# Performance work log

Hardware: AMD Instinct MI355X
Metric: run time of the kernel (lower is better)

Reference implementation:

```python
import jax, jax.numpy as jnp
import numpy as np

RANKS_HIGH = 15   # dt.RANKS.HIGH in the repo
SUITS_HIGH = 14   # padded so conv output last dim == 10 (Linear(10,32))
EPS = 1e-5


def _bn(x, g, b, axes):
    # Batch-norm over `axes` with channel dim = 1, training-mode batch stats.
    m = jnp.mean(x, axis=axes, keepdims=True)
    v = jnp.var(x, axis=axes, keepdims=True)
    xn = (x - m) * jax.lax.rsqrt(v + EPS)
    shp = [1] * x.ndim
    shp[1] = -1
    return xn * g.reshape(shp) + b.reshape(shp)


def setup_inputs() -> dict:
    key = jax.random.key(0)
    ks = jax.random.split(key, 16)
    M = 4096
    s = 0.05
    return {
        "x": jax.random.randint(ks[0], (M, 5, 2), 0, 4),  # (rank, suit) indices
        "conv_w": jax.random.normal(ks[1], (64, 5, 5, 5), jnp.float32) * s,
        "conv_b": jax.random.normal(ks[2], (64,), jnp.float32) * s,
        "bn0_g": jnp.ones((64,), jnp.float32),
        "bn0_b": jnp.zeros((64,), jnp.float32),
        "w_rank": jax.random.normal(ks[3], (32, 10), jnp.float32) * s,
        "b_rank": jax.random.normal(ks[4], (32,), jnp.float32) * s,
        "w_h1": jax.random.normal(ks[5], (32, 32), jnp.float32) * s,
        "b_h1": jax.random.normal(ks[6], (32,), jnp.float32) * s,
        "bn1_g": jnp.ones((64,), jnp.float32),
        "bn1_b": jnp.zeros((64,), jnp.float32),
        "w_h2": jax.random.normal(ks[7], (16, 32), jnp.float32) * s,
        "b_h2": jax.random.normal(ks[8], (16,), jnp.float32) * s,
        "bn2_g": jnp.ones((64,), jnp.float32),
        "bn2_b": jnp.zeros((64,), jnp.float32),
        "w_out": jax.random.normal(ks[9], (9, 11264), jnp.float32) * s,
        "b_out": jax.random.normal(ks[10], (9,), jnp.float32) * s,
    }


def reference(x, conv_w, conv_b, bn0_g, bn0_b, w_rank, b_rank, w_h1, b_h1,
              bn1_g, bn1_b, w_h2, b_h2, bn2_g, bn2_b, w_out, b_out):
    ranks = x[:, :, 0]
    suits = x[:, :, 1]
    # Vectorized replacement of the double Python-loop one-hot scatter:
    # three_d[j, i, ranks[j, i], suits[j, i]] = 1  ->  outer product of one-hots.
    three_d = (jax.nn.one_hot(ranks, RANKS_HIGH, dtype=jnp.float32)[..., :, None]
               * jax.nn.one_hot(suits, SUITS_HIGH, dtype=jnp.float32)[..., None, :])  # [M,5,15,14]
    r = jax.lax.conv_general_dilated(
        three_d, conv_w, window_strides=(1, 1), padding="VALID",
        dimension_numbers=("NCHW", "OIHW", "NCHW"))  # [M,64,11,10]
    r = r + conv_b[None, :, None, None]
    r = jax.nn.relu(_bn(r, bn0_g, bn0_b, (0, 2, 3)))
    r = jax.nn.relu(jnp.einsum("mchs,os->mcho", r, w_rank) + b_rank)      # [M,64,11,32]
    r = jnp.einsum("mchi,oi->mcho", r, w_h1) + b_h1                        # [M,64,11,32]
    r = jax.nn.relu(_bn(r, bn1_g, bn1_b, (0, 2, 3)))
    r = jnp.einsum("mchi,oi->mcho", r, w_h2) + b_h2                        # [M,64,11,16]
    r = jax.nn.relu(_bn(r, bn2_g, bn2_b, (0, 2, 3)))
    r = r.reshape(r.shape[0], -1)                                          # [M,11264]
    return r @ w_out.T + b_out                                             # [M,9]
```

## Files before the change

### kernel.cpp

```cpp
#include <hip/hip_runtime.h>
#include <hip/hip_bf16.h>

#define EPSV 1e-5f

typedef float vf2 __attribute__((ext_vector_type(2)));
typedef _Float16 h4f __attribute__((ext_vector_type(4)));
typedef _Float16 h8f __attribute__((ext_vector_type(8)));

__device__ __forceinline__ vf2 pk_fma(vf2 a, vf2 b, vf2 c) {
  vf2 d;
  asm("v_pk_fma_f32 %0, %1, %2, %3" : "=v"(d) : "v"(a), "v"(b), "v"(c));
  return d;
}
__device__ __forceinline__ vf2 pk_mul(vf2 a, vf2 b) {
  vf2 d;
  asm("v_pk_mul_f32 %0, %1, %2" : "=v"(d) : "v"(a), "v"(b));
  return d;
}

__device__ __forceinline__ void lds_barrier() {
  asm volatile("s_waitcnt lgkmcnt(0)" ::: "memory");
  __builtin_amdgcn_s_barrier();
}

#define CVT4(dst, base, v, al, be)                               \
  dst[base + 0].x = fmaxf(al * (float)v[0] + be, 0.f);           \
  dst[base + 0].y = fmaxf(al * (float)v[1] + be, 0.f);           \
  dst[base + 1].x = fmaxf(al * (float)v[2] + be, 0.f);           \
  dst[base + 1].y = fmaxf(al * (float)v[3] + be, 0.f);           \
  dst[base + 2].x = fmaxf(al * (float)v[4] + be, 0.f);           \
  dst[base + 2].y = fmaxf(al * (float)v[5] + be, 0.f);           \
  dst[base + 3].x = fmaxf(al * (float)v[6] + be, 0.f);           \
  dst[base + 3].y = fmaxf(al * (float)v[7] + be, 0.f);

#define WS_SUM0   0
#define WS_SSQ0   64
#define WS_SUM1   128
#define WS_SSQ1   192
#define WS_SUM2   256
#define WS_SSQ2   320
#define WS_AL0    384
#define WS_BE0    448
#define WS_ZBG    512
#define WS_T1BG   576
#define WS_AL1    2624
#define WS_BE1    2688
#define WS_T2BG   2752
#define WS_AL2    3776
#define WS_BE2    3840
#define WS_A2BG   3904
#define WS_OC     4928
#define WS_CU     4992
#define WS_CW     5120
#define WS_WSUM   10304
#define WS_HSL    19584
#define WS_T1     65536

#define CONV_LDS 5184
#define NHIST 2640

__device__ __forceinline__ void stage_conv(float* sW, const float* __restrict__ conv_w,
                                           int nthr) {
  for (int i = threadIdx.x; i < 8000; i += nthr) {
    int k = i / 125, rem = i - k * 125;
    int cc = rem / 25, r2 = rem - cc * 25;
    int di = r2 / 5, dj = r2 - di * 5;
    if (di < 4 && dj < 4) sW[k * 81 + cc * 16 + di * 4 + dj] = conv_w[i];
  }
  for (int k = threadIdx.x; k < 64; k += nthr) sW[k * 81 + 80] = 0.f;
}

__device__ __forceinline__ void stage_conv_fast(float* sW, const float* __restrict__ cw) {
  const float4* src = (const float4*)cw;
  float4* dst = (float4*)sW;
  for (int i = threadIdx.x; i < CONV_LDS / 4; i += 256) dst[i] = src[i];
}

__device__ __forceinline__ int conv_idx(int di, int dj, int cc) {
  int idx = cc * 16 + di * 4 + dj;
  return ((di | dj) >= 0) ? idx : 80;
}

__global__ __launch_bounds__(256) void k_prep3(
    const int* __restrict__ x, const float* __restrict__ conv_w,
    const float* __restrict__ w_out, float* __restrict__ ws, int M) {
  __shared__ float h[NHIST];
  const int b = blockIdx.x;
  const int tid = threadIdx.x;
  if (b < 8) {
    float* cw = ws + WS_CW;
    const int gid = b * 256 + tid;
    for (int i = gid; i < 8000; i += 8 * 256) {
      int k = i / 125, rem = i - k * 125;
      int cc = rem / 25, r2 = rem - cc * 25;
      int di = r2 / 5, dj = r2 - di * 5;
      if (di < 4 && dj < 4) cw[k * 81 + cc * 16 + di * 4 + dj] = conv_w[i];
    }
    for (int k = gid; k < 64; k += 8 * 256) cw[k * 81 + 80] = 0.f;
  } else if (b < 44) {
    const int gid = (b - 8) * 256 + tid;
    if (gid < 9216) {
      int j = gid / 1024, kp = gid - j * 1024;
      int k = kp >> 4, p = kp & 15;
      float s = 0.f;
#pragma unroll
      for (int yy = 4; yy < 11; ++yy)
        s += w_out[j * 11264 + k * 176 + yy * 16 + p];
      ws[WS_WSUM + gid] = s;
    }
  } else {
    const int slice = b - 44;
    for (int i = tid; i < NHIST; i += 256) h[i] = 0.f;
    __syncthreads();
    for (int m = slice * 256 + tid; m < M; m += 16 * 256) {
      int v[5];
      const int2* xp = (const int2*)(x + m * 10);
#pragma unroll
      for (int cc = 0; cc < 5; ++cc) {
        int2 t = xp[cc];
        v[cc] = (t.x << 2) | t.y;
      }
#pragma unroll
      for (int cc = 0; cc < 5; ++cc) atomicAdd(&h[cc * 16 + v[cc]], 1.f);
      int pr = 0;
#pragma unroll
      for (int a = 0; a < 5; ++a)
#pragma unroll
        for (int bb = a + 1; bb < 5; ++bb) {
          atomicAdd(&h[80 + pr * 256 + v[a] * 16 + v[bb]], 1.f);
          ++pr;
        }
    }
    __syncthreads();
    for (int i = tid; i < NHIST; i += 256)
      ws[WS_HSL + slice * NHIST + i] = h[i];
  }
}

__global__ __launch_bounds__(256) void k_stats0h(
    const float* __restrict__ conv_b, float* __restrict__ ws, int M) {
  __shared__ float sWk[81];
  __shared__ float sH[NHIST];
  __shared__ float sRed[8];
  const int tid = threadIdx.x;
  const int k = blockIdx.x;
  if (tid < 81) sWk[tid] = ws[WS_CW + k * 81 + tid];
  for (int i = tid; i < NHIST; i += 256) {
    float s = 0.f;
#pragma unroll
    for (int sl = 0; sl < 16; ++sl) s += ws[WS_HSL + sl * NHIST + i];
    sH[i] = s;
  }
  __syncthreads();
  const float cb = conv_b[k];
  float L = 0.f, Q = 0.f, P = 0.f;
  for (int it = tid; it < 1280; it += 256) {
    int pos = it / 80, rem = it - pos * 80;
    int cc = rem >> 4, v = rem & 15;
    int y = pos >> 2, xx = pos & 3;
    float w = sWk[conv_idx((v >> 2) - y, (v & 3) - xx, cc)];
    float n = sH[cc * 16 + v];
    L += n * w;
    Q += n * w * w;
  }
  if (tid < 160) {
    int pos = tid / 10, pr = tid - pos * 10;
    int y = pos >> 2, xx = pos & 3;
    int a, b;
    if (pr < 4)      { a = 0; b = pr + 1; }
    else if (pr < 7) { a = 1; b = pr - 2; }
    else if (pr < 9) { a = 2; b = pr - 4; }
    else             { a = 3; b = 4; }
    const float* Hp = sH + 80 + pr * 256;
    for (int v1 = 0; v1 < 16; ++v1) {
      float w1 = sWk[conv_idx((v1 >> 2) - y, (v1 & 3) - xx, a)];
      float acc = 0.f;
#pragma unroll
      for (int v2 = 0; v2 < 16; ++v2) {
        float w2 = sWk[conv_idx((v2 >> 2) - y, (v2 & 3) - xx, b)];
        acc += Hp[v1 * 16 + v2] * w2;
      }
      P += w1 * acc;
    }
  }
  float A = L, B = Q + 2.f * cb * L + 2.f * P;
  A += __shfl_xor(A, 1);  B += __shfl_xor(B, 1);
  A += __shfl_xor(A, 2);  B += __shfl_xor(B, 2);
  A += __shfl_xor(A, 4);  B += __shfl_xor(B, 4);
  A += __shfl_xor(A, 8);  B += __shfl_xor(B, 8);
  A += __shfl_xor(A, 16); B += __shfl_xor(B, 16);
  A += __shfl_xor(A, 32); B += __shfl_xor(B, 32);
  const int lane = tid & 63, wv = tid >> 6;
  if (lane == 0) { sRed[wv * 2] = A; sRed[wv * 2 + 1] = B; }
  __syncthreads();
  if (tid == 0) {
    float At = sRed[0] + sRed[2] + sRed[4] + sRed[6];
    float Bt = sRed[1] + sRed[3] + sRed[5] + sRed[7];
    const float a16 = 16.f * (float)M;
    ws[WS_SUM0 + k] = At + a16 * cb;
    ws[WS_SSQ0 + k] = Bt + a16 * cb * cb;
    ws[WS_SUM1 + k] = 0.f;
    ws[WS_SSQ1 + k] = 0.f;
    ws[WS_SUM2 + k] = 0.f;
    ws[WS_SSQ2 + k] = 0.f;
  }
}

__global__ __launch_bounds__(256) void k_t1(
    const int* __restrict__ x, const float* __restrict__ conv_b,
    const float* __restrict__ g0, const float* __restrict__ b0,
    const float* __restrict__ w_rank, const float* __restrict__ b_rank,
    const float* __restrict__ w_h1, const float* __restrict__ b_h1,
    float* __restrict__ ws, float* __restrict__ t1, int M) {
  __shared__ float sW[CONV_LDS];
  __shared__ float sCU[32];
  stage_conv_fast(sW, ws + WS_CW);
  if (threadIdx.x < 32) {
    float cuv = 0.f;
    for (int s2 = 4; s2 < 10; ++s2) cuv += w_rank[threadIdx.x * 10 + s2];
    sCU[threadIdx.x] = cuv;
  }
  __syncthreads();
  const int tid = threadIdx.x;
  const int y = tid & 3, k = tid >> 2;
  const float cb = conv_b[k];
  const float n0 = 110.f * (float)M;
  const float S0  = ws[WS_SUM0 + k] + 94.f * (float)M * cb;
  const float SS0 = ws[WS_SSQ0 + k] + 94.f * (float)M * cb * cb;
  const float mu0 = S0 / n0;
  const float var0 = SS0 / n0 - mu0 * mu0;
  const float al = rsqrtf(var0 + EPSV) * g0[k];
  const float be = b0[k] - mu0 * al;
  const float zbg = fmaxf(cb * al + be, 0.f);
  const float* Wk = &sW[k * 81];
  const vf2* wrp = (const vf2*)w_rank;
  const vf2* w1p = (const vf2*)w_h1;
  h8f* t1h8 = (h8f*)t1;
  float sAcc = 0.f, ssAcc = 0.f;
  const int NP = (M + 1) >> 1;
  for (int mp = blockIdx.x; mp < NP; mp += gridDim.x) {
    const int mA = mp * 2, mB = mA + 1;
    const bool hasB = (mB < M);
    const int mBs = hasB ? mB : mA;
    int rA[5], cA[5], rB[5], cBx[5];
    const int2* xpA = (const int2*)(x + mA * 10);
    const int2* xpB = (const int2*)(x + mBs * 10);
#pragma unroll
    for (int cc = 0; cc < 5; ++cc) {
      int2 tA = xpA[cc]; rA[cc] = tA.x; cA[cc] = tA.y;
      int2 tB = xpB[cc]; rB[cc] = tB.x; cBx[cc] = tB.y;
    }
    float a0A[4], a0B[4];
#pragma unroll
    for (int xx = 0; xx < 4; ++xx) {
      float vA = cb, vB = cb;
#pragma unroll
      for (int cc = 0; cc < 5; ++cc) {
        vA += Wk[conv_idx(rA[cc] - y, cA[cc] - xx, cc)];
        vB += Wk[conv_idx(rB[cc] - y, cBx[cc] - xx, cc)];
      }
      a0A[xx] = fmaxf(al * vA + be, 0.f);
      a0B[xx] = fmaxf(al * vB + be, 0.f);
    }
    vf2 aAp[2], aBp[2];
    aAp[0].x = a0A[0]; aAp[0].y = a0A[1];
    aAp[1].x = a0A[2]; aAp[1].y = a0A[3];
    aBp[0].x = a0B[0]; aBp[0].y = a0B[1];
    aBp[1].x = a0B[2]; aBp[1].y = a0B[3];
    __builtin_amdgcn_sched_barrier(0);
    vf2 r1A[16], r1B[16];
#pragma unroll
    for (int o2 = 0; o2 < 16; ++o2) {
      const int oa = 2 * o2, ob = oa + 1;
      vf2 w0 = wrp[oa * 5], w1 = wrp[oa * 5 + 1];
      vf2 w2 = wrp[ob * 5], w3 = wrp[ob * 5 + 1];
      const float basea = b_rank[oa] + zbg * sCU[oa];
      const float baseb = b_rank[ob] + zbg * sCU[ob];
      vf2 accAa = pk_mul(aAp[0], w0); accAa = pk_fma(aAp[1], w1, accAa);
      vf2 accAb = pk_mul(aAp[0], w2); accAb = pk_fma(aAp[1], w3, accAb);
      vf2 accBa = pk_mul(aBp[0], w0); accBa = pk_fma(aBp[1], w1, accBa);
      vf2 accBb = pk_mul(aBp[0], w2); accBb = pk_fma(aBp[1], w3, accBb);
      vf2 ra, rb;
      ra.x = fmaxf(basea + accAa.x + accAa.y, 0.f);
      ra.y = fmaxf(baseb + accAb.x + accAb.y, 0.f);
      rb.x = fmaxf(basea + accBa.x + accBa.y, 0.f);
      rb.y = fmaxf(baseb + accBb.x + accBb.y, 0.f);
      r1A[o2] = ra;
      r1B[o2] = rb;
    }
    __builtin_amdgcn_sched_barrier(0);
    float sBm = 0.f, ssBm = 0.f;
#pragma unroll
    for (int ch = 0; ch < 4; ++ch) {
      float accA[8], accB[8];
#pragma unroll
      for (int u = 0; u < 8; ++u) {
        const int o = ch * 8 + u;
        vf2 a2A = {0.f, 0.f}, a2B = {0.f, 0.f};
#pragma unroll
        for (int i = 0; i < 16; ++i) {
          vf2 w = w1p[o * 16 + i];
          a2A = pk_fma(r1A[i], w, a2A);
          a2B = pk_fma(r1B[i], w, a2B);
        }
        const float bb = b_h1[o];
        float aA = bb + a2A.x + a2A.y;
        float aB = bb + a2B.x + a2B.y;
        accA[u] = aA; accB[u] = aB;
        sAcc += aA; ssAcc += aA * aA;
        sBm += aB;  ssBm += aB * aB;
      }
      h8f stA;
#pragma unroll
      for (int u = 0; u < 8; ++u) stA[u] = (_Float16)accA[u];
      t1h8[((size_t)mA * 4 + ch) * 256 + tid] = stA;
      if (hasB) {
        h8f stB;
#pragma unroll
        for (int u = 0; u < 8; ++u) stB[u] = (_Float16)accB[u];
        t1h8[((size_t)mB * 4 + ch) * 256 + tid] = stB;
      }
      __builtin_amdgcn_sched_barrier(0);
    }
    if (hasB) { sAcc += sBm; ssAcc += ssBm; }
  }
  sAcc  += __shfl_xor(sAcc, 1);  sAcc  += __shfl_xor(sAcc, 2);
  ssAcc += __shfl_xor(ssAcc, 1); ssAcc += __shfl_xor(ssAcc, 2);
  if (y == 0) {
    atomicAdd(&ws[WS_SUM1 + k], sAcc);
    atomicAdd(&ws[WS_SSQ1 + k], ssAcc);
  }
}

__global__ __launch_bounds__(256) void k_t2(
    const float* __restrict__ conv_b, const float* __restrict__ g0,
    const float* __restrict__ b0, const float* __restrict__ w_rank,
    const float* __restrict__ b_rank, const float* __restrict__ w_h1,
    const float* __restrict__ b_h1, const float* __restrict__ g1,
    const float* __restrict__ b1, const float* __restrict__ w_h2,
    const float* __restrict__ b_h2, float* __restrict__ ws,
    float* __restrict__ t1, int M) {
  __shared__ float sS[32];
  __shared__ float sWh1[1024];
  const int tid = threadIdx.x;
  for (int i = tid; i < 1024; i += 256) sWh1[i] = w_h1[i];
  if (tid < 32) {
    float s = 0.f;
    for (int s2 = 0; s2 < 10; ++s2) s += w_rank[tid * 10 + s2];
    sS[tid] = s;
  }
  __syncthreads();
  const int y = tid & 3, k = tid >> 2;
  const float fM = (float)M;
  const float cb = conv_b[k];
  const float n0 = 110.f * fM;
  const float S0  = ws[WS_SUM0 + k] + 94.f * fM * cb;
  const float SS0 = ws[WS_SSQ0 + k] + 94.f * fM * cb * cb;
  const float mu0 = S0 / n0;
  const float al0 = rsqrtf(SS0 / n0 - mu0 * mu0 + EPSV) * g0[k];
  const float be0 = b0[k] - mu0 * al0;
  const float zbg = fmaxf(cb * al0 + be0, 0.f);
  float r1bg[32];
#pragma unroll
  for (int o = 0; o < 32; ++o) r1bg[o] = fmaxf(zbg * sS[o] + b_rank[o], 0.f);
  float sb = 0.f, ssb = 0.f;
#pragma unroll
  for (int u = 0; u < 8; ++u) {
    const int o = y * 8 + u;
    float a = b_h1[o];
#pragma unroll
    for (int i = 0; i < 32; ++i) a += r1bg[i] * sWh1[o * 32 + i];
    sb += a;
    ssb += a * a;
  }
  sb  += __shfl_xor(sb, 1);  sb  += __shfl_xor(sb, 2);
  ssb += __shfl_xor(ssb, 1); ssb += __shfl_xor(ssb, 2);
  const float n1 = fM * 11.f * 32.f;
  const float S1  = ws[WS_SUM1 + k] + 7.f * fM * sb;
  const float SS1 = ws[WS_SSQ1 + k] + 7.f * fM * ssb;
  const float mu1 = S1 / n1;
  const float al1 = rsqrtf(SS1 / n1 - mu1 * mu1 + EPSV) * g1[k];
  const float be1 = b1[k] - mu1 * al1;
  const vf2* w2p = (const vf2*)w_h2;
  h8f* t1h8 = (h8f*)t1;
  float sAcc = 0.f, ssAcc = 0.f;
  const int NP = (M + 1) >> 1;
  const int G = gridDim.x;
  int mp = blockIdx.x;
  h8f cA0, cA1, cA2, cA3, cB0, cB1, cB2, cB3;
  h8f nA0, nA1, nA2, nA3, nB0, nB1, nB2, nB3;
  if (mp < NP) {
    const int mA = mp * 2;
    const int mBs = (mA + 1 < M) ? mA + 1 : mA;
    cA0 = t1h8[((size_t)mA * 4 + 0) * 256 + tid];
    cA1 = t1h8[((size_t)mA * 4 + 1) * 256 + tid];
    cA2 = t1h8[((size_t)mA * 4 + 2) * 256 + tid];
    cA3 = t1h8[((size_t)mA * 4 + 3) * 256 + tid];
    cB0 = t1h8[((size_t)mBs * 4 + 0) * 256 + tid];
    cB1 = t1h8[((size_t)mBs * 4 + 1) * 256 + tid];
    cB2 = t1h8[((size_t)mBs * 4 + 2) * 256 + tid];
    cB3 = t1h8[((size_t)mBs * 4 + 3) * 256 + tid];
  }
  while (mp < NP) {
    const int mA = mp * 2, mB = mA + 1;
    const bool hasB = (mB < M);
    const int mpn = mp + G;
    if (mpn < NP) {
      const int mAn = mpn * 2;
      const int mBn = (mAn + 1 < M) ? mAn + 1 : mAn;
      nA0 = t1h8[((size_t)mAn * 4 + 0) * 256 + tid];
      nA1 = t1h8[((size_t)mAn * 4 + 1) * 256 + tid];
      nA2 = t1h8[((size_t)mAn * 4 + 2) * 256 + tid];
      nA3 = t1h8[((size_t)mAn * 4 + 3) * 256 + tid];
      nB0 = t1h8[((size_t)mBn * 4 + 0) * 256 + tid];
      nB1 = t1h8[((size_t)mBn * 4 + 1) * 256 + tid];
      nB2 = t1h8[((size_t)mBn * 4 + 2) * 256 + tid];
      nB3 = t1h8[((size_t)mBn * 4 + 3) * 256 + tid];
    }
    vf2 a1A[16], a1B[16];
    CVT4(a1A, 0,  cA0, al1, be1);
    CVT4(a1A, 4,  cA1, al1, be1);
    CVT4(a1A, 8,  cA2, al1, be1);
    CVT4(a1A, 12, cA3, al1, be1);
    CVT4(a1B, 0,  cB0, al1, be1);
    CVT4(a1B, 4,  cB1, al1, be1);
    CVT4(a1B, 8,  cB2, al1, be1);
    CVT4(a1B, 12, cB3, al1, be1);
    float sBm = 0.f, ssBm = 0.f;
#pragma unroll
    for (int pv2 = 0; pv2 < 2; ++pv2) {
      float accA[8], accB[8];
#pragma unroll
      for (int u = 0; u < 8; ++u) {
        const int p = pv2 * 8 + u;
        vf2 a2A = {0.f, 0.f}, a2B = {0.f, 0.f};
#pragma unroll
        for (int i = 0; i < 16; ++i) {
          vf2 w = w2p[p * 16 + i];
          a2A = pk_fma(a1A[i], w, a2A);
          a2B = pk_fma(a1B[i], w, a2B);
        }
        const float bb = b_h2[p];
        float aA = bb + a2A.x + a2A.y;
        float aB = bb + a2B.x + a2B.y;
        accA[u] = aA; accB[u] = aB;
        sAcc += aA; ssAcc += aA * aA;
        sBm += aB;  ssBm += aB * aB;
      }
      h8f stA;
#pragma unroll
      for (int u = 0; u < 8; ++u) stA[u] = (_Float16)accA[u];
      t1h8[((size_t)mA * 4 + pv2) * 256 + tid] = stA;
      if (hasB) {
        h8f stB;
#pragma unroll
        for (int u = 0; u < 8; ++u) stB[u] = (_Float16)accB[u];
        t1h8[((size_t)mB * 4 + pv2) * 256 + tid] = stB;
      }
    }
    if (hasB) { sAcc += sBm; ssAcc += ssBm; }
    mp = mpn;
    if (mp < NP) {
      cA0 = nA0; cA1 = nA1; cA2 = nA2; cA3 = nA3;
      cB0 = nB0; cB1 = nB1; cB2 = nB2; cB3 = nB3;
    }
  }
  sAcc  += __shfl_xor(sAcc, 1);  sAcc  += __shfl_xor(sAcc, 2);
  ssAcc += __shfl_xor(ssAcc, 1); ssAcc += __shfl_xor(ssAcc, 2);
  if (y == 0) {
    atomicAdd(&ws[WS_SUM2 + k], sAcc);
    atomicAdd(&ws[WS_SSQ2 + k], ssAcc);
  }
}

__global__ __launch_bounds__(256) void k_fin2p(
    const float* __restrict__ conv_b, const float* __restrict__ g0,
    const float* __restrict__ b0, const float* __restrict__ w_rank,
    const float* __restrict__ b_rank, const float* __restrict__ w_h1,
    const float* __restrict__ b_h1, const float* __restrict__ g1,
    const float* __restrict__ b1, const float* __restrict__ w_h2,
    const float* __restrict__ b_h2, const float* __restrict__ g2,
    const float* __restrict__ b2, const float* __restrict__ b_out,
    float* __restrict__ ws, int M) {
  __shared__ float sS[32];
  __shared__ float sWh1[1024];
  __shared__ float sWh2[512];
  __shared__ float sWs[9216];
  __shared__ float sA2[1024];
  __shared__ float red[576];
  const int tid = threadIdx.x;
  for (int i = tid; i < 1024; i += 256) sWh1[i] = w_h1[i];
  for (int i = tid; i < 512; i += 256) sWh2[i] = w_h2[i];
  for (int i = tid; i < 9216; i += 256) sWs[i] = ws[WS_WSUM + i];
  if (tid < 32) {
    float s = 0.f;
    for (int s2 = 0; s2 < 10; ++s2) s += w_rank[tid * 10 + s2];
    sS[tid] = s;
  }
  __syncthreads();
  const int k = tid >> 2, q = tid & 3;
  const float fM = (float)M;
  const float cb = conv_b[k];
  const float n0 = 110.f * fM;
  const float S0  = ws[WS_SUM0 + k] + 94.f * fM * cb;
  const float SS0 = ws[WS_SSQ0 + k] + 94.f * fM * cb * cb;
  const float mu0 = S0 / n0;
  const float al0 = rsqrtf(SS0 / n0 - mu0 * mu0 + EPSV) * g0[k];
  const float be0 = b0[k] - mu0 * al0;
  const float zbg = fmaxf(cb * al0 + be0, 0.f);
  float r1bg[32];
#pragma unroll
  for (int o = 0; o < 32; ++o) r1bg[o] = fmaxf(zbg * sS[o] + b_rank[o], 0.f);
  float t1bg[8];
  float sb = 0.f, ssb = 0.f;
#pragma unroll
  for (int u = 0; u < 8; ++u) {
    const int o = q * 8 + u;
    float a = b_h1[o];
#pragma unroll
    for (int i = 0; i < 32; ++i) a += r1bg[i] * sWh1[o * 32 + i];
    t1bg[u] = a;
    sb += a;
    ssb += a * a;
  }
  sb  += __shfl_xor(sb, 1);  sb  += __shfl_xor(sb, 2);
  ssb += __shfl_xor(ssb, 1); ssb += __shfl_xor(ssb, 2);
  const float n1 = fM * 11.f * 32.f;
  const float S1  = ws[WS_SUM1 + k] + 7.f * fM * sb;
  const float SS1 = ws[WS_SSQ1 + k] + 7.f * fM * ssb;
  const float mu1 = S1 / n1;
  const float al1 = rsqrtf(SS1 / n1 - mu1 * mu1 + EPSV) * g1[k];
  const float be1 = b1[k] - mu1 * al1;
  float a1bg[8];
#pragma unroll
  for (int u = 0; u < 8; ++u) a1bg[u] = fmaxf(al1 * t1bg[u] + be1, 0.f);
  float pt[16];
#pragma unroll
  for (int p = 0; p < 16; ++p) {
    float a = 0.f;
#pragma unroll
    for (int u = 0; u < 8; ++u) a += a1bg[u] * sWh2[p * 32 + q * 8 + u];
    pt[p] = a;
  }
#pragma unroll
  for (int p = 0; p < 16; ++p) {
    pt[p] += __shfl_xor(pt[p], 1);
    pt[p] += __shfl_xor(pt[p], 2);
  }
  float sb2 = 0.f, ssb2 = 0.f;
#pragma unroll
  for (int p = 0; p < 16; ++p) {
    float v = pt[p] + b_h2[p];
    pt[p] = v;
    sb2 += v;
    ssb2 += v * v;
  }
  const float n2 = fM * 11.f * 16.f;
  const float S2  = ws[WS_SUM2 + k] + 7.f * fM * sb2;
  const float SS2 = ws[WS_SSQ2 + k] + 7.f * fM * ssb2;
  const float mu2 = S2 / n2;
  const float al2 = rsqrtf(SS2 / n2 - mu2 * mu2 + EPSV) * g2[k];
  const float be2 = b2[k] - mu2 * al2;
  if (q == 0) {
    ws[WS_AL2 + k] = al2;
    ws[WS_BE2 + k] = be2;
  }
#pragma unroll
  for (int v2 = 0; v2 < 4; ++v2) {
    const int p = q * 4 + v2;
    sA2[k * 16 + p] = fmaxf(al2 * pt[p] + be2, 0.f);
  }
  __syncthreads();
  for (int u = tid; u < 576; u += 256) {
    const int kk = u / 9, j = u - kk * 9;
    float acc = 0.f;
#pragma unroll
    for (int p = 0; p < 16; ++p)
      acc += sA2[kk * 16 + p] * sWs[j * 1024 + kk * 16 + p];
    red[u] = acc;
  }
  __syncthreads();
  if (tid < 9) {
    float acc = b_out[tid];
    for (int t = 0; t < 64; ++t) acc += red[t * 9 + tid];
    ws[WS_OC + tid] = acc;
  }
}

__global__ __launch_bounds__(256) void k_out(
    const float* __restrict__ w_out, const float* __restrict__ ws,
    const float* __restrict__ t1, float* __restrict__ out, int M) {
  __shared__ float sOC[9];
  __shared__ float sP[256][19];
  __shared__ float sR2[18 * 8];
  if (threadIdx.x < 9) sOC[threadIdx.x] = ws[WS_OC + threadIdx.x];
  const int tid = threadIdx.x;
  const int y = tid & 3, k = tid >> 2;
  const float al2 = ws[WS_AL2 + k], be2 = ws[WS_BE2 + k];
  const float4* wo = (const float4*)(w_out + k * 176 + y * 16);
  const h8f* t2h8 = (const h8f*)t1;
  const int NP = (M + 1) >> 1;
  const int G = gridDim.x;
  int mp = blockIdx.x;
  h8f cA0, cA1, cB0, cB1, nA0, nA1, nB0, nB1;
  if (mp < NP) {
    const int mA = mp * 2;
    const int mBs = (mA + 1 < M) ? mA + 1 : mA;
    cA0 = t2h8[((size_t)mA * 4 + 0) * 256 + tid];
    cA1 = t2h8[((size_t)mA * 4 + 1) * 256 + tid];
    cB0 = t2h8[((size_t)mBs * 4 + 0) * 256 + tid];
    cB1 = t2h8[((size_t)mBs * 4 + 1) * 256 + tid];
  }
  bool first = true;
  while (mp < NP) {
    const int mA = mp * 2, mB = mA + 1;
    const bool hasB = (mB < M);
    const int mpn = mp + G;
    if (mpn < NP) {
      const int mAn = mpn * 2;
      const int mBn = (mAn + 1 < M) ? mAn + 1 : mAn;
      nA0 = t2h8[((size_t)mAn * 4 + 0) * 256 + tid];
      nA1 = t2h8[((size_t)mAn * 4 + 1) * 256 + tid];
      nB0 = t2h8[((size_t)mBn * 4 + 0) * 256 + tid];
      nB1 = t2h8[((size_t)mBn * 4 + 1) * 256 + tid];
    }
    vf2 a2A[8], a2B[8];
    CVT4(a2A, 0, cA0, al2, be2);
    CVT4(a2A, 4, cA1, al2, be2);
    CVT4(a2B, 0, cB0, al2, be2);
    CVT4(a2B, 4, cB1, al2, be2);
    if (!first) lds_barrier();
    first = false;
#pragma unroll
    for (int j = 0; j < 9; ++j) {
      float4 w0 = wo[j * 2816 + 0], w1 = wo[j * 2816 + 1];
      float4 w2 = wo[j * 2816 + 2], w3 = wo[j * 2816 + 3];
      vf2 aA = {0.f, 0.f}, aB = {0.f, 0.f};
      vf2 t;
      t.x = w0.x; t.y = w0.y; aA = pk_fma(a2A[0], t, aA); aB = pk_fma(a2B[0], t, aB);
      t.x = w0.z; t.y = w0.w; aA = pk_fma(a2A[1], t, aA); aB = pk_fma(a2B[1], t, aB);
      t.x = w1.x; t.y = w1.y; aA = pk_fma(a2A[2], t, aA); aB = pk_fma(a2B[2], t, aB);
      t.x = w1.z; t.y = w1.w; aA = pk_fma(a2A[3], t, aA); aB = pk_fma(a2B[3], t, aB);
      t.x = w2.x; t.y = w2.y; aA = pk_fma(a2A[4], t, aA); aB = pk_fma(a2B[4], t, aB);
      t.x = w2.z; t.y = w2.w; aA = pk_fma(a2A[5], t, aA); aB = pk_fma(a2B[5], t, aB);
      t.x = w3.x; t.y = w3.y; aA = pk_fma(a2A[6], t, aA); aB = pk_fma(a2B[6], t, aB);
      t.x = w3.z; t.y = w3.w; aA = pk_fma(a2A[7], t, aA); aB = pk_fma(a2B[7], t, aB);
      sP[tid][j] = aA.x + aA.y;
      sP[tid][9 + j] = aB.x + aB.y;
    }
    lds_barrier();
    if (tid < 144) {
      const int slot = tid / 8, part = tid & 7;
      float s = 0.f;
#pragma unroll 8
      for (int t = 0; t < 32; ++t) s += sP[part + t * 8][slot];
      sR2[slot * 8 + part] = s;
    }
    lds_barrier();
    if (tid < 18) {
      float s = 0.f;
#pragma unroll
      for (int p8 = 0; p8 < 8; ++p8) s += sR2[tid * 8 + p8];
      if (tid < 9) out[mA * 9 + tid] = sOC[tid] + s;
      else if (hasB) out[mB * 9 + (tid - 9)] = sOC[tid - 9] + s;
    }
    mp = mpn;
    if (mp < NP) {
      cA0 = nA0; cA1 = nA1; cB0 = nB0; cB1 = nB1;
    }
  }
}

__global__ __launch_bounds__(64) void k_fin0(
    const float* __restrict__ conv_b, const float* __restrict__ g0,
    const float* __restrict__ b0, const float* __restrict__ w_rank,
    const float* __restrict__ b_rank, const float* __restrict__ w_h1,
    const float* __restrict__ b_h1, float* __restrict__ ws, int M) {
  __shared__ float sS[32];
  const int t = threadIdx.x;
  if (t < 32) {
    float su = 0.f;
    for (int s2 = 0; s2 < 10; ++s2) su += w_rank[t * 10 + s2];
    sS[t] = su;
    float cu = 0.f;
    for (int s2 = 4; s2 < 10; ++s2) cu += w_rank[t * 10 + s2];
    ws[WS_CU + t] = cu;
  }
  __syncthreads();
  const int k = t;
  const float n0 = 110.f * (float)M;
  const float cb = conv_b[k];
  const float S  = ws[WS_SUM0 + k] + 94.f * (float)M * cb;
  const float SS = ws[WS_SSQ0 + k] + 94.f * (float)M * cb * cb;
  const float mu = S / n0;
  const float var = SS / n0 - mu * mu;
  const float rstd = rsqrtf(var + EPSV);
  const float al = rstd * g0[k];
  const float be = b0[k] - mu * al;
  ws[WS_AL0 + k] = al;
  ws[WS_BE0 + k] = be;
  const float zbg = fmaxf(cb * al + be, 0.f);
  ws[WS_ZBG + k] = zbg;
  float r1bg[32];
#pragma unroll
  for (int o = 0; o < 32; ++o) r1bg[o] = fmaxf(zbg * sS[o] + b_rank[o], 0.f);
  float sb = 0.f, ssb = 0.f;
  for (int o = 0; o < 32; ++o) {
    float acc = b_h1[o];
#pragma unroll
    for (int i = 0; i < 32; ++i) acc += r1bg[i] * w_h1[o * 32 + i];
    ws[WS_T1BG + k * 32 + o] = acc;
    sb += acc;
    ssb += acc * acc;
  }
  ws[WS_SUM1 + k] = 7.f * (float)M * sb;
  ws[WS_SSQ1 + k] = 7.f * (float)M * ssb;
}

__global__ __launch_bounds__(64) void k_fin1(
    const float* __restrict__ g1, const float* __restrict__ b1,
    const float* __restrict__ w_h2, const float* __restrict__ b_h2,
    float* __restrict__ ws, int M) {
  const int k = threadIdx.x;
  const float n1 = (float)M * 11.f * 32.f;
  const float S = ws[WS_SUM1 + k], SS = ws[WS_SSQ1 + k];
  const float mu = S / n1;
  const float var = SS / n1 - mu * mu;
  const float rstd = rsqrtf(var + EPSV);
  const float al = rstd * g1[k];
  const float be = b1[k] - mu * al;
  ws[WS_AL1 + k] = al;
  ws[WS_BE1 + k] = be;
  float a1bg[32];
#pragma unroll
  for (int o = 0; o < 32; ++o)
    a1bg[o] = fmaxf(al * ws[WS_T1BG + k * 32 + o] + be, 0.f);
  float sb = 0.f, ssb = 0.f;
  for (int p = 0; p < 16; ++p) {
    float acc = b_h2[p];
#pragma unroll
    for (int o = 0; o < 32; ++o) acc += a1bg[o] * w_h2[p * 32 + o];
    ws[WS_T2BG + k * 16 + p] = acc;
    sb += acc;
    ssb += acc * acc;
  }
  ws[WS_SUM2 + k] = 7.f * (float)M * sb;
  ws[WS_SSQ2 + k] = 7.f * (float)M * ssb;
}

__global__ __launch_bounds__(256) void k_stats0(
    const int* __restrict__ x, const float* __restrict__ conv_w,
    const float* __restrict__ conv_b, float* __restrict__ ws, int M) {
  __shared__ float sW[CONV_LDS];
  stage_conv(sW, conv_w, 256);
  __syncthreads();
  const int tid = threadIdx.x;
  const int mg = tid & 3;
  const int k  = tid >> 2;
  const float cb = conv_b[k];
  const float* Wk = &sW[k * 81];
  float s = 0.f, ss = 0.f;
  for (int m = blockIdx.x * 4 + mg; m < M; m += gridDim.x * 4) {
    int r[5], c[5];
    const int2* xp = (const int2*)(x + m * 10);
#pragma unroll
    for (int cc = 0; cc < 5; ++cc) { int2 t = xp[cc]; r[cc] = t.x; c[cc] = t.y; }
#pragma unroll
    for (int y = 0; y < 4; ++y) {
#pragma unroll
      for (int xx = 0; xx < 4; ++xx) {
        float v = cb;
#pragma unroll
        for (int cc = 0; cc < 5; ++cc)
          v += Wk[conv_idx(r[cc] - y, c[cc] - xx, cc)];
        s += v;
        ss += v * v;
      }
      __builtin_amdgcn_sched_barrier(0);
    }
  }
  s  += __shfl_xor(s, 1);  s  += __shfl_xor(s, 2);
  ss += __shfl_xor(ss, 1); ss += __shfl_xor(ss, 2);
  if (mg == 0) {
    atomicAdd(&ws[WS_SUM0 + k], s);
    atomicAdd(&ws[WS_SSQ0 + k], ss);
  }
}

__global__ __launch_bounds__(256) void k_stats1(
    const int* __restrict__ x, const float* __restrict__ conv_w,
    const float* __restrict__ conv_b, const float* __restrict__ w_rank,
    const float* __restrict__ b_rank, const float* __restrict__ w_h1,
    const float* __restrict__ b_h1, float* __restrict__ ws, int M) {
  __shared__ float sW[CONV_LDS];
  stage_conv(sW, conv_w, 256);
  __syncthreads();
  const int tid = threadIdx.x;
  const int y = tid & 3, k = tid >> 2;
  const float cb = conv_b[k];
  const float al = ws[WS_AL0 + k], be = ws[WS_BE0 + k], zbg = ws[WS_ZBG + k];
  const float* Wk = &sW[k * 81];
  const float* cu = ws + WS_CU;
  float sAcc = 0.f, ssAcc = 0.f;
  for (int m = blockIdx.x; m < M; m += gridDim.x) {
    int r[5], c[5];
    const int2* xp = (const int2*)(x + m * 10);
#pragma unroll
    for (int cc = 0; cc < 5; ++cc) { int2 t = xp[cc]; r[cc] = t.x; c[cc] = t.y; }
    float a0[4];
#pragma unroll
    for (int xx = 0; xx < 4; ++xx) {
      float v = cb;
#pragma unroll
      for (int cc = 0; cc < 5; ++cc)
        v += Wk[conv_idx(r[cc] - y, c[cc] - xx, cc)];
      a0[xx] = fmaxf(al * v + be, 0.f);
    }
    __builtin_amdgcn_sched_barrier(0);
    float r1[32];
#pragma unroll
    for (int o = 0; o < 32; ++o) {
      float acc = b_rank[o] + zbg * cu[o];
#pragma unroll
      for (int xx = 0; xx < 4; ++xx) acc += a0[xx] * w_rank[o * 10 + xx];
      r1[o] = fmaxf(acc, 0.f);
    }
    __builtin_amdgcn_sched_barrier(0);
    float s1 = 0.f, ss1 = 0.f;
#pragma unroll
    for (int ch = 0; ch < 4; ++ch) {
#pragma unroll
      for (int u = 0; u < 8; ++u) {
        const int o = ch * 8 + u;
        float acc = b_h1[o];
#pragma unroll
        for (int i = 0; i < 32; ++i) acc += r1[i] * w_h1[o * 32 + i];
        s1 += acc;
        ss1 += acc * acc;
      }
      __builtin_amdgcn_sched_barrier(0);
    }
    sAcc += s1;
    ssAcc += ss1;
  }
  sAcc  += __shfl_xor(sAcc, 1);  sAcc  += __shfl_xor(sAcc, 2);
  ssAcc += __shfl_xor(ssAcc, 1); ssAcc += __shfl_xor(ssAcc, 2);
  if (y == 0) {
    atomicAdd(&ws[WS_SUM1 + k], sAcc);
    atomicAdd(&ws[WS_SSQ1 + k], ssAcc);
  }
}

__global__ __launch_bounds__(256) void k_stats2(
    const int* __restrict__ x, const float* __restrict__ conv_w,
    const float* __restrict__ conv_b, const float* __restrict__ w_rank,
    const float* __restrict__ b_rank, const float* __restrict__ w_h1,
    const float* __restrict__ b_h1, const float* __restrict__ w_h2,
    const float* __restrict__ b_h2, float* __restrict__ ws, int M) {
  __shared__ float sW[CONV_LDS];
  stage_conv(sW, conv_w, 256);
  __syncthreads();
  const int tid = threadIdx.x;
  const int y = tid & 3, k = tid >> 2;
  const float cb = conv_b[k];
  const float al = ws[WS_AL0 + k], be = ws[WS_BE0 + k], zbg = ws[WS_ZBG + k];
  const float al1 = ws[WS_AL1 + k], be1 = ws[WS_BE1 + k];
  const float* Wk = &sW[k * 81];
  const float* cu = ws + WS_CU;
  float sAcc = 0.f, ssAcc = 0.f;
  for (int m = blockIdx.x; m < M; m += gridDim.x) {
    int r[5], c[5];
    const int2* xp = (const int2*)(x + m * 10);
#pragma unroll
    for (int cc = 0; cc < 5; ++cc) { int2 t = xp[cc]; r[cc] = t.x; c[cc] = t.y; }
    float a0[4];
#pragma unroll
    for (int xx = 0; xx < 4; ++xx) {
      float v = cb;
#pragma unroll
      for (int cc = 0; cc < 5; ++cc)
        v += Wk[conv_idx(r[cc] - y, c[cc] - xx, cc)];
      a0[xx] = fmaxf(al * v + be, 0.f);
    }
    __builtin_amdgcn_sched_barrier(0);
    float r1[32];
#pragma unroll
    for (int o = 0; o < 32; ++o) {
      float acc = b_rank[o] + zbg * cu[o];
#pragma unroll
      for (int xx = 0; xx < 4; ++xx) acc += a0[xx] * w_rank[o * 10 + xx];
      r1[o] = fmaxf(acc, 0.f);
    }
    __builtin_amdgcn_sched_barrier(0);
    float t2[16];
#pragma unroll
    for (int p = 0; p < 16; ++p) t2[p] = b_h2[p];
#pragma unroll
    for (int ch = 0; ch < 4; ++ch) {
      float a1c[8];
#pragma unroll
      for (int u = 0; u < 8; ++u) {
        const int o = ch * 8 + u;
        float acc = b_h1[o];
#pragma unroll
        for (int i = 0; i < 32; ++i) acc += r1[i] * w_h1[o * 32 + i];
        a1c[u] = fmaxf(al1 * acc + be1, 0.f);
      }
      __builtin_amdgcn_sched_barrier(0);
#pragma unroll
      for (int p = 0; p < 16; ++p) {
        float acc = t2[p];
#pragma unroll
        for (int u = 0; u < 8; ++u) acc += a1c[u] * w_h2[p * 32 + ch * 8 + u];
        t2[p] = acc;
      }
      __builtin_amdgcn_sched_barrier(0);
    }
    float s2l = 0.f, ss2l = 0.f;
#pragma unroll
    for (int p = 0; p < 16; ++p) { s2l += t2[p]; ss2l += t2[p] * t2[p]; }
    sAcc += s2l;
    ssAcc += ss2l;
  }
  sAcc  += __shfl_xor(sAcc, 1);  sAcc  += __shfl_xor(sAcc, 2);
  ssAcc += __shfl_xor(ssAcc, 1); ssAcc += __shfl_xor(ssAcc, 2);
  if (y == 0) {
    atomicAdd(&ws[WS_SUM2 + k], sAcc);
    atomicAdd(&ws[WS_SSQ2 + k], ssAcc);
  }
}

__global__ __launch_bounds__(64) void k_fin2(
    const float* __restrict__ g2, const float* __restrict__ b2,
    const float* __restrict__ w_out, const float* __restrict__ b_out,
    float* __restrict__ ws, int M) {
  __shared__ float red[64 * 9];
  const int k = threadIdx.x;
  const float n2 = (float)M * 11.f * 16.f;
  const float S = ws[WS_SUM2 + k], SS = ws[WS_SSQ2 + k];
  const float mu = S / n2;
  const float var = SS / n2 - mu * mu;
  const float rstd = rsqrtf(var + EPSV);
  const float al = rstd * g2[k];
  const float be = b2[k] - mu * al;
  ws[WS_AL2 + k] = al;
  ws[WS_BE2 + k] = be;
  float a2bg[16];
#pragma unroll
  for (int p = 0; p < 16; ++p)
    a2bg[p] = fmaxf(al * ws[WS_T2BG + k * 16 + p] + be, 0.f);
  for (int j = 0; j < 9; ++j) {
    float acc = 0.f;
#pragma unroll
    for (int p = 0; p < 16; ++p) {
      float wsum = 0.f;
#pragma unroll
      for (int yy = 4; yy < 11; ++yy)
        wsum += w_out[j * 11264 + k * 176 + yy * 16 + p];
      acc += a2bg[p] * wsum;
    }
    red[k * 9 + j] = acc;
  }
  __syncthreads();
  if (k < 9) {
    float acc = b_out[k];
    for (int t = 0; t < 64; ++t) acc += red[t * 9 + k];
    ws[WS_OC + k] = acc;
  }
}

__global__ __launch_bounds__(256) void k_final(
    const int* __restrict__ x, const float* __restrict__ conv_w,
    const float* __restrict__ conv_b, const float* __restrict__ w_rank,
    const float* __restrict__ b_rank, const float* __restrict__ w_h1,
    const float* __restrict__ b_h1, const float* __restrict__ w_h2,
    const float* __restrict__ b_h2, const float* __restrict__ w_out,
    const float* __restrict__ ws, float* __restrict__ out, int M) {
  __shared__ float sW[CONV_LDS];
  __shared__ float sOC[9];
  __shared__ float sRed[4][9];
  stage_conv(sW, conv_w, 256);
  if (threadIdx.x < 9) sOC[threadIdx.x] = ws[WS_OC + threadIdx.x];
  __syncthreads();
  const int tid = threadIdx.x;
  const int lane = tid & 63, wv = tid >> 6;
  const int y = tid & 3, k = tid >> 2;
  const float cb = conv_b[k];
  const float al = ws[WS_AL0 + k], be = ws[WS_BE0 + k], zbg = ws[WS_ZBG + k];
  const float al1 = ws[WS_AL1 + k], be1 = ws[WS_BE1 + k];
  const float al2 = ws[WS_AL2 + k], be2 = ws[WS_BE2 + k];
  const float* Wk = &sW[k * 81];
  const float* cu = ws + WS_CU;
  const float4* wo = (const float4*)(w_out + k * 176 + y * 16);
  bool first = true;
  for (int m = blockIdx.x; m < M; m += gridDim.x) {
    if (!first) __syncthreads();
    first = false;
    int r[5], c[5];
    const int2* xp = (const int2*)(x + m * 10);
#pragma unroll
    for (int cc = 0; cc < 5; ++cc) { int2 t = xp[cc]; r[cc] = t.x; c[cc] = t.y; }
    float a0[4];
#pragma unroll
    for (int xx = 0; xx < 4; ++xx) {
      float v = cb;
#pragma unroll
      for (int cc = 0; cc < 5; ++cc)
        v += Wk[conv_idx(r[cc] - y, c[cc] - xx, cc)];
      a0[xx] = fmaxf(al * v + be, 0.f);
    }
    __builtin_amdgcn_sched_barrier(0);
    float r1[32];
#pragma unroll
    for (int o = 0; o < 32; ++o) {
      float acc = b_rank[o] + zbg * cu[o];
#pragma unroll
      for (int xx = 0; xx < 4; ++xx) acc += a0[xx] * w_rank[o * 10 + xx];
      r1[o] = fmaxf(acc, 0.f);
    }
    __builtin_amdgcn_sched_barrier(0);
    float t2[16];
#pragma unroll
    for (int p = 0; p < 16; ++p) t2[p] = b_h2[p];
#pragma unroll
    for (int ch = 0; ch < 4; ++ch) {
      float a1c[8];
#pragma unroll
      for (int u = 0; u < 8; ++u) {
        const int o = ch * 8 + u;
        float acc = b_h1[o];
#pragma unroll
        for (int i = 0; i < 32; ++i) acc += r1[i] * w_h1[o * 32 + i];
        a1c[u] = fmaxf(al1 * acc + be1, 0.f);
      }
      __builtin_amdgcn_sched_barrier(0);
#pragma unroll
      for (int p = 0; p < 16; ++p) {
        float acc = t2[p];
#pragma unroll
        for (int u = 0; u < 8; ++u) acc += a1c[u] * w_h2[p * 32 + ch * 8 + u];
        t2[p] = acc;
      }
      __builtin_amdgcn_sched_barrier(0);
    }
    float a2[16];
#pragma unroll
    for (int p = 0; p < 16; ++p) a2[p] = fmaxf(al2 * t2[p] + be2, 0.f);
    float po[9];
#pragma unroll
    for (int j = 0; j < 9; ++j) {
      float4 w0 = wo[j * 2816 + 0], w1 = wo[j * 2816 + 1];
      float4 w2 = wo[j * 2816 + 2], w3 = wo[j * 2816 + 3];
      po[j] = a2[0] * w0.x + a2[1] * w0.y + a2[2] * w0.z + a2[3] * w0.w
            + a2[4] * w1.x + a2[5] * w1.y + a2[6] * w1.z + a2[7] * w1.w
            + a2[8] * w2.x + a2[9] * w2.y + a2[10] * w2.z + a2[11] * w2.w
            + a2[12] * w3.x + a2[13] * w3.y + a2[14] * w3.z + a2[15] * w3.w;
    }
#pragma unroll
    for (int j = 0; j < 9; ++j) {
      float v = po[j];
      v += __shfl_xor(v, 1);
      v += __shfl_xor(v, 2);
      v += __shfl_xor(v, 4);
      v += __shfl_xor(v, 8);
      v += __shfl_xor(v, 16);
      v += __shfl_xor(v, 32);
      po[j] = v;
    }
    if (lane == 0) {
#pragma unroll
      for (int j = 0; j < 9; ++j) sRed[wv][j] = po[j];
    }
    __syncthreads();
    if (tid < 9) {
      float acc = sOC[tid];
#pragma unroll
      for (int w2i = 0; w2i < 4; ++w2i) acc += sRed[w2i][tid];
      out[m * 9 + tid] = acc;
    }
  }
}

extern "C" void kernel_launch(void* const* d_in, const int* in_sizes, int n_in,
                              void* d_out, int out_size, void* d_ws, size_t ws_size,
                              hipStream_t stream) {
  const int*   x      = (const int*)d_in[0];
  const float* conv_w = (const float*)d_in[1];
  const float* conv_b = (const float*)d_in[2];
  const float* bn0_g  = (const float*)d_in[3];
  const float* bn0_b  = (const float*)d_in[4];
  const float* w_rank = (const float*)d_in[5];
  const float* b_rank = (const float*)d_in[6];
  const float* w_h1   = (const float*)d_in[7];
  const float* b_h1   = (const float*)d_in[8];
  const float* bn1_g  = (const float*)d_in[9];
  const float* bn1_b  = (const float*)d_in[10];
  const float* w_h2   = (const float*)d_in[11];
  const float* b_h2   = (const float*)d_in[12];
  const float* bn2_g  = (const float*)d_in[13];
  const float* bn2_b  = (const float*)d_in[14];
  const float* w_out  = (const float*)d_in[15];
  const float* b_out  = (const float*)d_in[16];
  float* out = (float*)d_out;
  float* ws  = (float*)d_ws;
  const int M = in_sizes[0] / 10;
  const size_t need = ((size_t)WS_T1 + (size_t)M * 4096) * sizeof(float);
  const int NP = (M + 1) >> 1;
  const int gridt = NP < 2048 ? NP : 2048;
  const int grid2 = NP < 512 ? NP : 512;

  if (ws_size >= need) {
    float* t1 = ws + WS_T1;
    k_prep3<<<60, 256, 0, stream>>>(x, conv_w, w_out, ws, M);
    k_stats0h<<<64, 256, 0, stream>>>(conv_b, ws, M);
    k_t1<<<gridt, 256, 0, stream>>>(x, conv_b, bn0_g, bn0_b, w_rank, b_rank,
                                    w_h1, b_h1, ws, t1, M);
    k_t2<<<grid2, 256, 0, stream>>>(conv_b, bn0_g, bn0_b, w_rank, b_rank,
                                    w_h1, b_h1, bn1_g, bn1_b, w_h2, b_h2,
                                    ws, t1, M);
    k_fin2p<<<1, 256, 0, stream>>>(conv_b, bn0_g, bn0_b, w_rank, b_rank,
                                   w_h1, b_h1, bn1_g, bn1_b, w_h2, b_h2,
                                   bn2_g, bn2_b, b_out, ws, M);
    k_out<<<grid2, 256, 0, stream>>>(w_out, ws, t1, out, M);
  } else {
    hipMemsetAsync(ws, 0, 384 * sizeof(float), stream);
    k_stats0<<<512, 256, 0, stream>>>(x, conv_w, conv_b, ws, M);
    k_fin0<<<1, 64, 0, stream>>>(conv_b, bn0_g, bn0_b, w_rank, b_rank, w_h1, b_h1, ws, M);
    k_stats1<<<1024, 256, 0, stream>>>(x, conv_w, conv_b, w_rank, b_rank, w_h1, b_h1,
                                       ws, M);
    k_fin1<<<1, 64, 0, stream>>>(bn1_g, bn1_b, w_h2, b_h2, ws, M);
    k_stats2<<<1024, 256, 0, stream>>>(x, conv_w, conv_b, w_rank, b_rank, w_h1, b_h1,
                                       w_h2, b_h2, ws, M);
    k_fin2<<<1, 64, 0, stream>>>(bn2_g, bn2_b, w_out, b_out, ws, M);
    k_final<<<1024, 256, 0, stream>>>(x, conv_w, conv_b, w_rank, b_rank, w_h1, b_h1,
                                      w_h2, b_h2, w_out, ws, out, M);
  }
}
```

Baseline: 274.4 us.

## Use fp16 dot2 for the h1 layer and process four samples per iteration

k_t1 now packs the ReLU'd rank-layer outputs into fp16 pairs and computes the w_h1 projection with v_dot2_f32_f16 against an fp16 copy of w_h1 staged in LDS. Each loop iteration handles four samples instead of two, so every weight load is reused across more samples, and the grid is halved to match. This lowers the FMA instruction count and the global weight traffic, at the cost of fp16 rounding on the intermediate activations and weights and higher register pressure.

```diff
diff --git a/kernel.cpp b/kernel.cpp
--- a/kernel.cpp
+++ b/kernel.cpp
@@ -15,6 +15,16 @@
 __device__ __forceinline__ vf2 pk_mul(vf2 a, vf2 b) {
   vf2 d;
   asm("v_pk_mul_f32 %0, %1, %2" : "=v"(d) : "v"(a), "v"(b));
+  return d;
+}
+
+__device__ __forceinline__ unsigned int pkh(float a, float b) {
+  auto v = __builtin_amdgcn_cvt_pkrtz(a, b);
+  return __builtin_bit_cast(unsigned int, v);
+}
+__device__ __forceinline__ float dot2h(unsigned int a, unsigned int b, float c) {
+  float d;
+  asm("v_dot2_f32_f16 %0, %1, %2, %3" : "=v"(d) : "v"(a), "v"(b), "v"(c));
   return d;
 }
 
@@ -213,8 +223,16 @@
     const float* __restrict__ w_h1, const float* __restrict__ b_h1,
     float* __restrict__ ws, float* __restrict__ t1, int M) {
   __shared__ float sW[CONV_LDS];
+  __shared__ unsigned int sWh1h[512];
   __shared__ float sCU[32];
   stage_conv_fast(sW, ws + WS_CW);
+  {
+    const vf2* src = (const vf2*)w_h1;
+    for (int i = threadIdx.x; i < 512; i += 256) {
+      vf2 v = src[i];
+      sWh1h[i] = pkh(v.x, v.y);
+    }
+  }
   if (threadIdx.x < 32) {
     float cuv = 0.f;
     for (int s2 = 4; s2 < 10; ++s2) cuv += w_rank[threadIdx.x * 10 + s2];
@@ -234,41 +252,36 @@
   const float zbg = fmaxf(cb * al + be, 0.f);
   const float* Wk = &sW[k * 81];
   const vf2* wrp = (const vf2*)w_rank;
-  const vf2* w1p = (const vf2*)w_h1;
   h8f* t1h8 = (h8f*)t1;
   float sAcc = 0.f, ssAcc = 0.f;
-  const int NP = (M + 1) >> 1;
-  for (int mp = blockIdx.x; mp < NP; mp += gridDim.x) {
-    const int mA = mp * 2, mB = mA + 1;
-    const bool hasB = (mB < M);
-    const int mBs = hasB ? mB : mA;
-    int rA[5], cA[5], rB[5], cBx[5];
-    const int2* xpA = (const int2*)(x + mA * 10);
-    const int2* xpB = (const int2*)(x + mBs * 10);
-#pragma unroll
-    for (int cc = 0; cc < 5; ++cc) {
-      int2 tA = xpA[cc]; rA[cc] = tA.x; cA[cc] = tA.y;
-      int2 tB = xpB[cc]; rB[cc] = tB.x; cBx[cc] = tB.y;
-    }
-    float a0A[4], a0B[4];
-#pragma unroll
-    for (int xx = 0; xx < 4; ++xx) {
-      float vA = cb, vB = cb;
-#pragma unroll
-      for (int cc = 0; cc < 5; ++cc) {
-        vA += Wk[conv_idx(rA[cc] - y, cA[cc] - xx, cc)];
-        vB += Wk[conv_idx(rB[cc] - y, cBx[cc] - xx, cc)];
-      }
-      a0A[xx] = fmaxf(al * vA + be, 0.f);
-      a0B[xx] = fmaxf(al * vB + be, 0.f);
-    }
-    vf2 aAp[2], aBp[2];
-    aAp[0].x = a0A[0]; aAp[0].y = a0A[1];
-    aAp[1].x = a0A[2]; aAp[1].y = a0A[3];
-    aBp[0].x = a0B[0]; aBp[0].y = a0B[1];
-    aBp[1].x = a0B[2]; aBp[1].y = a0B[3];
+  const int NQ = (M + 3) >> 2;
+  for (int q4 = blockIdx.x; q4 < NQ; q4 += gridDim.x) {
+    const int m0 = q4 * 4;
+    int mI[4]; bool hv[4];
+#pragma unroll
+    for (int j = 0; j < 4; ++j) {
+      hv[j] = (m0 + j < M);
+      mI[j] = hv[j] ? m0 + j : m0;
+    }
+    vf2 ap[4][2];
+#pragma unroll
+    for (int j = 0; j < 4; ++j) {
+      int rr[5], cl[5];
+      const int2* xp = (const int2*)(x + mI[j] * 10);
+#pragma unroll
+      for (int cc = 0; cc < 5; ++cc) { int2 t = xp[cc]; rr[cc] = t.x; cl[cc] = t.y; }
+#pragma unroll
+      for (int xx = 0; xx < 4; ++xx) {
+        float v = cb;
+#pragma unroll
+        for (int cc = 0; cc < 5; ++cc)
+          v += Wk[conv_idx(rr[cc] - y, cl[cc] - xx, cc)];
+        float a = fmaxf(al * v + be, 0.f);
+        if (xx < 2) ap[j][0][xx] = a; else ap[j][1][xx - 2] = a;
+      }
+    }
     __builtin_amdgcn_sched_barrier(0);
-    vf2 r1A[16], r1B[16];
+    unsigned int r1[4][16];
 #pragma unroll
     for (int o2 = 0; o2 < 16; ++o2) {
       const int oa = 2 * o2, ob = oa + 1;
@@ -276,53 +289,51 @@
       vf2 w2 = wrp[ob * 5], w3 = wrp[ob * 5 + 1];
       const float basea = b_rank[oa] + zbg * sCU[oa];
       const float baseb = b_rank[ob] + zbg * sCU[ob];
-      vf2 accAa = pk_mul(aAp[0], w0); accAa = pk_fma(aAp[1], w1, accAa);
-      vf2 accAb = pk_mul(aAp[0], w2); accAb = pk_fma(aAp[1], w3, accAb);
-      vf2 accBa = pk_mul(aBp[0], w0); accBa = pk_fma(aBp[1], w1, accBa);
-      vf2 accBb = pk_mul(aBp[0], w2); accBb = pk_fma(aBp[1], w3, accBb);
-      vf2 ra, rb;
-      ra.x = fmaxf(basea + accAa.x + accAa.y, 0.f);
-      ra.y = fmaxf(baseb + accAb.x + accAb.y, 0.f);
-      rb.x = fmaxf(basea + accBa.x + accBa.y, 0.f);
-      rb.y = fmaxf(baseb + accBb.x + accBb.y, 0.f);
-      r1A[o2] = ra;
-      r1B[o2] = rb;
+#pragma unroll
+      for (int j = 0; j < 4; ++j) {
+        vf2 aa = pk_mul(ap[j][0], w0); aa = pk_fma(ap[j][1], w1, aa);
+        vf2 ab = pk_mul(ap[j][0], w2); ab = pk_fma(ap[j][1], w3, ab);
+        float ra = fmaxf(basea + aa.x + aa.y, 0.f);
+        float rb = fmaxf(baseb + ab.x + ab.y, 0.f);
+        r1[j][o2] = pkh(ra, rb);
+      }
     }
     __builtin_amdgcn_sched_barrier(0);
-    float sBm = 0.f, ssBm = 0.f;
 #pragma unroll
     for (int ch = 0; ch < 4; ++ch) {
-      float accA[8], accB[8];
+      float acc[4][8];
 #pragma unroll
       for (int u = 0; u < 8; ++u) {
         const int o = ch * 8 + u;
-        vf2 a2A = {0.f, 0.f}, a2B = {0.f, 0.f};
+        float a0_ = 0.f, a1_ = 0.f, a2_ = 0.f, a3_ = 0.f;
 #pragma unroll
         for (int i = 0; i < 16; ++i) {
-          vf2 w = w1p[o * 16 + i];
-          a2A = pk_fma(r1A[i], w, a2A);
-          a2B = pk_fma(r1B[i], w, a2B);
+          unsigned int w = sWh1h[o * 16 + i];
+          a0_ = dot2h(r1[0][i], w, a0_);
+          a1_ = dot2h(r1[1][i], w, a1_);
+          a2_ = dot2h(r1[2][i], w, a2_);
+          a3_ = dot2h(r1[3][i], w, a3_);
         }
         const float bb = b_h1[o];
-        float aA = bb + a2A.x + a2A.y;
-        float aB = bb + a2B.x + a2B.y;
-        accA[u] = aA; accB[u] = aB;
-        sAcc += aA; ssAcc += aA * aA;
-        sBm += aB;  ssBm += aB * aB;
-      }
-      h8f stA;
-#pragma unroll
-      for (int u = 0; u < 8; ++u) stA[u] = (_Float16)accA[u];
-      t1h8[((size_t)mA * 4 + ch) * 256 + tid] = stA;
-      if (hasB) {
-        h8f stB;
-#pragma unroll
-        for (int u = 0; u < 8; ++u) stB[u] = (_Float16)accB[u];
-        t1h8[((size_t)mB * 4 + ch) * 256 + tid] = stB;
+        acc[0][u] = a0_ + bb; acc[1][u] = a1_ + bb;
+        acc[2][u] = a2_ + bb; acc[3][u] = a3_ + bb;
+      }
+#pragma unroll
+      for (int j = 0; j < 4; ++j) {
+        if (hv[j]) {
+          h8f st;
+#pragma unroll
+          for (int u = 0; u < 8; ++u) st[u] = (_Float16)acc[j][u];
+          t1h8[((size_t)mI[j] * 4 + ch) * 256 + tid] = st;
+#pragma unroll
+          for (int u = 0; u < 8; ++u) {
+            sAcc += acc[j][u];
+            ssAcc += acc[j][u] * acc[j][u];
+          }
+        }
       }
       __builtin_amdgcn_sched_barrier(0);
     }
-    if (hasB) { sAcc += sBm; ssAcc += ssBm; }
   }
   sAcc  += __shfl_xor(sAcc, 1);  sAcc  += __shfl_xor(sAcc, 2);
   ssAcc += __shfl_xor(ssAcc, 1); ssAcc += __shfl_xor(ssAcc, 2);
@@ -1106,14 +1117,15 @@
   const int M = in_sizes[0] / 10;
   const size_t need = ((size_t)WS_T1 + (size_t)M * 4096) * sizeof(float);
   const int NP = (M + 1) >> 1;
-  const int gridt = NP < 2048 ? NP : 2048;
+  const int NQ = (M + 3) >> 2;
+  const int gridq = NQ < 1024 ? NQ : 1024;
   const int grid2 = NP < 512 ? NP : 512;
 
   if (ws_size >= need) {
     float* t1 = ws + WS_T1;
     k_prep3<<<60, 256, 0, stream>>>(x, conv_w, w_out, ws, M);
     k_stats0h<<<64, 256, 0, stream>>>(conv_b, ws, M);
-    k_t1<<<gridt, 256, 0, stream>>>(x, conv_b, bn0_g, bn0_b, w_rank, b_rank,
+    k_t1<<<gridq, 256, 0, stream>>>(x, conv_b, bn0_g, bn0_b, w_rank, b_rank,
                                     w_h1, b_h1, ws, t1, M);
     k_t2<<<grid2, 256, 0, stream>>>(conv_b, bn0_g, bn0_b, w_rank, b_rank,
                                     w_h1, b_h1, bn1_g, bn1_b, w_h2, b_h2,
```

After: 253.4 us. -7.7%, faster.
